# Optimization experiments

Measured on AMD Instinct MI355X. Metric: run time of the kernel, lower is better.

## Reference

```python
import jax, jax.numpy as jnp
import numpy as np


def _patch_points(P):
    # replicates: meshgrid(y,x,z, indexing='ij'); points = cat([zz, yy, xx], -1).reshape(-1,3)
    lin = jnp.linspace(-1.0, 1.0, P)
    a, b, c = jnp.meshgrid(lin, lin, lin, indexing='ij')  # all identical linspaces
    pts = jnp.stack([c, b, a], axis=-1).reshape(-1, 3)     # (P^3, 3)
    return pts


def _proj_locations(points, angles):
    # Tomographic projection geometry (generate_projections_location):
    # rotate points about the detector-vertical axis and keep in-plane coords.
    # points: (N,3); angles: (A,) radians. Returns (A, N, 2) grid coords (x, y)
    # in grid_sample convention (last dim: x indexes width, y indexes height).
    p0 = points[:, 0]
    p1 = points[:, 1]
    p2 = points[:, 2]
    c = jnp.cos(angles)[:, None]   # (A,1)
    s = jnp.sin(angles)[:, None]
    gx = p0[None, :] * c + p2[None, :] * s          # (A, N)
    gy = jnp.broadcast_to(p1[None, :], gx.shape)    # (A, N)
    return jnp.stack([gx, gy], axis=-1)             # (A, N, 2)


def _bilinear_sample(img, grid):
    # img: (C,H,W); grid: (N,2) in [-1,1], align_corners=True, padding zeros.
    C, H, W = img.shape
    ix = (grid[:, 0] + 1.0) * 0.5 * (W - 1)
    iy = (grid[:, 1] + 1.0) * 0.5 * (H - 1)
    ix0 = jnp.floor(ix)
    iy0 = jnp.floor(iy)
    ix1 = ix0 + 1.0
    iy1 = iy0 + 1.0
    wx1 = ix - ix0
    wx0 = 1.0 - wx1
    wy1 = iy - iy0
    wy0 = 1.0 - wy1

    def corner(iyc, ixc, w):
        valid = (ixc >= 0) & (ixc <= W - 1) & (iyc >= 0) & (iyc <= H - 1)
        xi = jnp.clip(ixc, 0, W - 1).astype(jnp.int32)
        yi = jnp.clip(iyc, 0, H - 1).astype(jnp.int32)
        return img[:, yi, xi] * (w * valid)[None, :]   # (C,N)

    return (corner(iy0, ix0, wy0 * wx0) + corner(iy0, ix1, wy0 * wx1)
            + corner(iy1, ix0, wy1 * wx0) + corner(iy1, ix1, wy1 * wx1))


def setup_inputs() -> dict:
    key = jax.random.key(0)
    k1, k2 = jax.random.split(key)
    B, A, P = 128, 121, 33
    x = jax.random.normal(k1, (B, A, P, P), dtype=jnp.float32)
    angles = jax.random.uniform(k2, (1, A), dtype=jnp.float32,
                                minval=0.0, maxval=2.0 * np.pi)
    return {"x": x, "angles": angles}


def reference(x, angles):
    B, A, P, _ = x.shape
    pts = _patch_points(P)                       # (P^3, 3)
    grids = _proj_locations(pts, angles[0])      # (A, P^3, 2)
    xs = jnp.transpose(x, (1, 0, 2, 3))          # (A, B, P, P)

    def body(acc, inp):
        xi, gi = inp                             # (B,P,P), (P^3,2)
        return acc + _bilinear_sample(xi, gi), None

    acc0 = jnp.zeros((B, P * P * P), dtype=x.dtype)
    acc, _ = jax.lax.scan(body, acc0, (xs, grids))
    x_fbp = acc.reshape(B, P, P, P) / A
    return x_fbp
```

## Files before the change

kernel.cpp:

```cpp
#include <hip/hip_runtime.h>
#include <hip/hip_fp16.h>
#include <math.h>


#define PDIM 33
#define PP   1089
#define A_   121
#define K_   3993
#define KP   4032
#define MP   1152
#define MT2  18
#define NT2  66
#define OUTB 35937

typedef _Float16 f16x8 __attribute__((ext_vector_type(8)));
typedef float    f32x4 __attribute__((ext_vector_type(4)));

typedef __attribute__((address_space(1))) const unsigned int* gp_t;
typedef __attribute__((address_space(3))) unsigned int*       lp_t;


__global__ __launch_bounds__(128)
void wfill_kernel(const float* __restrict__ angles, __half* __restrict__ W)
{
    const int n = blockIdx.x;
    const int t = threadIdx.x;
    __half* row = W + (size_t)n * KP;
    for (int e = t; e < KP; e += 128) row[e] = __float2half_rn(0.0f);
    __syncthreads();
    if (n >= PP || t >= A_) return;
    const int j  = t;
    const int i0 = n / PDIM;
    const int i2 = n - i0 * PDIM;
    float s, c;
    sincosf(angles[j], &s, &c);
    float ix = fmaf((float)(i2 - 16), c, fmaf((float)(i0 - 16), s, 16.0f));
    float fl = floorf(ix);
    int   k0 = (int)fl;
    float w1 = ix - fl;
    float w0 = 1.0f - w1;
    __half* seg = row + j * PDIM;
    if (k0 >= 0     && k0 < PDIM)     seg[k0]     = __float2half_rn(w0);
    if (k0 + 1 >= 0 && k0 + 1 < PDIM) seg[k0 + 1] = __float2half_rn(w1);
}

__global__ __launch_bounds__(256)
void xt_kernel(const float* __restrict__ x, __half* __restrict__ Xt)
{
    const int n  = blockIdx.x;
    const int i1 = n >> 7;
    const int b  = n & 127;
    const float* src = x + (size_t)b * (A_ * PP) + (size_t)i1 * PDIM;
    unsigned int* dst = (unsigned int*)(Xt + (size_t)n * KP);
    for (int e = threadIdx.x; e < KP / 2; e += 256) {
        int kk0 = 2 * e, kk1 = 2 * e + 1;
        float v0 = 0.0f, v1 = 0.0f;
        if (kk0 < K_) {
            int j = kk0 / PDIM, k = kk0 - j * PDIM;
            v0 = src[(size_t)j * PP + k];
        }
        if (kk1 < K_) {
            int j = kk1 / PDIM, k = kk1 - j * PDIM;
            v1 = src[(size_t)j * PP + k];
        }
        dst[e] = __builtin_bit_cast(unsigned int,
                     __builtin_amdgcn_cvt_pkrtz(v0, v1));
    }
}

__global__ __launch_bounds__(256)
void gemm_kernel(const __half* __restrict__ W, const __half* __restrict__ Xt,
                 float* __restrict__ out, float invA)
{
    __shared__ _Float16 As[64 * 64];
    __shared__ _Float16 Bs[64 * 64];

    const int blk   = blockIdx.x;
    const int tileN = blk / MT2;
    const int tileM = blk - tileN * MT2;
    const int t     = threadIdx.x;
    const int lane  = t & 63;
    const int wave  = t >> 6;
    const int warpM = wave >> 1;
    const int warpN = wave & 1;
    const int quad  = lane >> 4;
    const int l15   = lane & 15;

    f32x4 acc[2][2] = {};

    const __half* Ab = W  + (size_t)(tileM * 64) * KP;
    const __half* Bb = Xt + (size_t)(tileN * 64) * KP;

    int srow[2], ssego[2];
#pragma unroll
    for (int i = 0; i < 2; ++i) {
        int cidx = t + i * 256;
        int row  = cidx >> 3;
        int seg  = cidx & 7;
        srow[i]  = row;
        ssego[i] = (seg ^ (row & 7)) * 8;
    }

    int arow[2], brow[2];
#pragma unroll
    for (int s = 0; s < 2; ++s) {
        arow[s] = warpM * 32 + s * 16 + l15;
        brow[s] = warpN * 32 + s * 16 + l15;
    }

    for (int kb = 0; kb < KP; kb += 64) {
        __syncthreads();
#pragma unroll
        for (int i = 0; i < 2; ++i) {
            const __half* ga = Ab + (size_t)srow[i] * KP + kb + ssego[i];
            const __half* gb = Bb + (size_t)srow[i] * KP + kb + ssego[i];
            __builtin_amdgcn_global_load_lds((gp_t)(const void*)ga,
                (lp_t)(void*)&As[(t + i * 256) * 8], 16, 0, 0);
            __builtin_amdgcn_global_load_lds((gp_t)(const void*)gb,
                (lp_t)(void*)&Bs[(t + i * 256) * 8], 16, 0, 0);
        }
        __syncthreads();

        f16x8 af[2][2], bf[2][2];
#pragma unroll
        for (int h = 0; h < 2; ++h) {
#pragma unroll
            for (int s = 0; s < 2; ++s) {
                int ks = h * 4 + quad;
                af[h][s] = *(const f16x8*)&As[arow[s] * 64 + ((ks ^ (arow[s] & 7)) * 8)];
                bf[h][s] = *(const f16x8*)&Bs[brow[s] * 64 + ((ks ^ (brow[s] & 7)) * 8)];
            }
        }
#pragma unroll
        for (int h = 0; h < 2; ++h)
#pragma unroll
            for (int ms = 0; ms < 2; ++ms)
#pragma unroll
                for (int ns = 0; ns < 2; ++ns)
                    acc[ms][ns] = __builtin_amdgcn_mfma_f32_16x16x32_f16(
                        af[h][ms], bf[h][ns], acc[ms][ns], 0, 0, 0);
    }

#pragma unroll
    for (int ns = 0; ns < 2; ++ns) {
        int nglob = tileN * 64 + warpN * 32 + ns * 16 + l15;
        int i1 = nglob >> 7;
        int b  = nglob & 127;
        float* ob = out + (size_t)b * OUTB + (size_t)i1 * PDIM;
#pragma unroll
        for (int ms = 0; ms < 2; ++ms) {
#pragma unroll
            for (int r = 0; r < 4; ++r) {
                int m = tileM * 64 + warpM * 32 + ms * 16 + quad * 4 + r;
                if (m < PP) {
                    int i0 = m / PDIM;
                    int i2 = m - i0 * PDIM;
                    ob[(size_t)i0 * PP + i2] = acc[ms][ns][r] * invA;
                }
            }
        }
    }
}


#define ROWW 47
#define PADL 7
#define BLK  384
#define NV   3
#define GRID 1280

typedef _Float16 h2v __attribute__((ext_vector_type(2)));

#if defined(__has_builtin)
#if __has_builtin(__builtin_amdgcn_fractf)
#define FRACTF(x) __builtin_amdgcn_fractf(x)
#endif
#endif
#ifndef FRACTF
#define FRACTF(x) ((x) - floorf(x))
#endif

__device__ __forceinline__ float fdot2u(unsigned int a, unsigned int b, float c)
{
    return __builtin_amdgcn_fdot2(__builtin_bit_cast(h2v, a),
                                  __builtin_bit_cast(h2v, b), c, false);
}

__global__ __launch_bounds__(BLK)
void fbp_adjoint_kernel(const float* __restrict__ x,
                        const float* __restrict__ angles,
                        float* __restrict__ out,
                        int nslice, float invA)
{
    __shared__ unsigned int dr[A_ * ROWW];
    __shared__ float2       cs_lds[A_];

    const int t = threadIdx.x;
    for (int j = t; j < A_; j += BLK) {
        float s, c;
        sincosf(angles[j], &s, &c);
        cs_lds[j] = make_float2(c, s);
    }

    float u0[NV], u2[NV];
#pragma unroll
    for (int nn = 0; nn < NV; ++nn) {
        int n  = t + nn * BLK;
        int nc = (n < PP) ? n : (PP - 1);
        int q0 = nc / PDIM;
        int q2 = nc - q0 * PDIM;
        u0[nn] = (float)(q0 - 16);
        u2[nn] = (float)(q2 - 16);
    }

    for (int slice = blockIdx.x; slice < nslice; slice += GRID) {
        if (slice != (int)blockIdx.x) __syncthreads();
        const int hb = slice / PDIM;
        const int i1 = slice - hb * PDIM;
        const int b0 = 2 * hb;
        const float* r0 = x + (size_t)b0 * (A_ * PP) + (size_t)i1 * PDIM;
        const float* r1 = r0 + (size_t)(A_ * PP);
        for (int e = t; e < A_ * ROWW; e += BLK) {
            int j = e / ROWW;
            int p = e - j * ROWW;
            int k = p - PADL;
            float f0 = 0.0f, f1 = 0.0f;
            if (k >= 0 && k < PDIM) {
                size_t o = (size_t)j * PP + k;
                f0 = r0[o];
                f1 = r1[o];
            }
            dr[e] = __builtin_bit_cast(unsigned int,
                        __halves2half2(__float2half_rn(f0), __float2half_rn(f1)));
        }
        __syncthreads();

        float a0[NV] = {0.0f, 0.0f, 0.0f};
        float a1[NV] = {0.0f, 0.0f, 0.0f};
#pragma unroll 2
        for (int j = 0; j < A_; ++j) {
            float2 cj = cs_lds[j];
            const unsigned int* base = &dr[j * ROWW];
#pragma unroll
            for (int nn = 0; nn < NV; ++nn) {
                float ixp = fmaf(u2[nn], cj.x, fmaf(u0[nn], cj.y, 23.0f));
                int   kp  = (int)ixp;
                float w1  = FRACTF(ixp);
                unsigned int wp = __builtin_bit_cast(unsigned int,
                                    __builtin_amdgcn_cvt_pkrtz(1.0f - w1, w1));
                unsigned int d0 = base[kp];
                unsigned int d1 = base[kp + 1];
                unsigned int p0 = __builtin_amdgcn_perm(d1, d0, 0x05040100u);
                unsigned int p1 = __builtin_amdgcn_perm(d1, d0, 0x07060302u);
                a0[nn] = fdot2u(p0, wp, a0[nn]);
                a1[nn] = fdot2u(p1, wp, a1[nn]);
            }
        }

        float* ob0 = out + (size_t)b0 * OUTB + (size_t)i1 * PDIM;
        float* ob1 = ob0 + (size_t)OUTB;
#pragma unroll
        for (int nn = 0; nn < NV; ++nn) {
            int n = t + nn * BLK;
            if (n < PP) {
                int q0 = n / PDIM;
                int q2 = n - q0 * PDIM;
                size_t o = (size_t)q0 * PP + q2;
                ob0[o] = a0[nn] * invA;
                ob1[o] = a1[nn] * invA;
            }
        }
    }
}


extern "C" void kernel_launch(void* const* d_in, const int* in_sizes, int n_in,
                              void* d_out, int out_size, void* d_ws, size_t ws_size,
                              hipStream_t stream)
{
    const float* x      = (const float*)d_in[0];
    const float* angles = (const float*)d_in[1];
    float* out          = (float*)d_out;

    const int A = in_sizes[1];
    const int B = in_sizes[0] / (A * PP);
    const float invA = 1.0f / (float)A;

    const size_t wBytes  = (size_t)MP * KP * sizeof(__half);
    const size_t xtBytes = (size_t)(PDIM * B) * KP * sizeof(__half);

    if (ws_size >= wBytes + xtBytes && A == A_ && B == 128) {
        __half* W  = (__half*)d_ws;
        __half* Xt = (__half*)((char*)d_ws + wBytes);
        wfill_kernel<<<MP, 128, 0, stream>>>(angles, W);
        xt_kernel<<<PDIM * B, 256, 0, stream>>>(x, Xt);
        gemm_kernel<<<NT2 * MT2, 256, 0, stream>>>(W, Xt, out, invA);
    } else {
        const int nslice = (B / 2) * PDIM;
        dim3 grid(GRID < nslice ? GRID : nslice);
        fbp_adjoint_kernel<<<grid, BLK, 0, stream>>>(x, angles, out,
                                                     nslice, invA);
    }
}
```

Before: 191.5 us.

## Fuse prep kernels into one launch and swizzle GEMM tiles across XCDs

Merges the weight-fill and input-transpose kernels into a single prep launch, with 256 threads per block and zeroing done in 16-byte stores, which saves one launch and its gap. Remaps GEMM workgroup IDs so each XCD gets a contiguous group of tiles made of clusters sharing M/N rows, aiming for better L2 reuse of W and Xt. The mapping is hardcoded for 1188 workgroups split over 8 XCDs, which ties it to this problem shape.

```diff
diff --git a/kernel.cpp b/kernel.cpp
--- a/kernel.cpp
+++ b/kernel.cpp
@@ -11,6 +11,7 @@
 #define MP   1152
 #define MT2  18
 #define NT2  66
+#define NWG  1188
 #define OUTB 35937
 
 typedef _Float16 f16x8 __attribute__((ext_vector_type(8)));
@@ -20,51 +21,54 @@
 typedef __attribute__((address_space(3))) unsigned int*       lp_t;
 
 
-__global__ __launch_bounds__(128)
-void wfill_kernel(const float* __restrict__ angles, __half* __restrict__ W)
-{
-    const int n = blockIdx.x;
-    const int t = threadIdx.x;
-    __half* row = W + (size_t)n * KP;
-    for (int e = t; e < KP; e += 128) row[e] = __float2half_rn(0.0f);
-    __syncthreads();
-    if (n >= PP || t >= A_) return;
-    const int j  = t;
-    const int i0 = n / PDIM;
-    const int i2 = n - i0 * PDIM;
-    float s, c;
-    sincosf(angles[j], &s, &c);
-    float ix = fmaf((float)(i2 - 16), c, fmaf((float)(i0 - 16), s, 16.0f));
-    float fl = floorf(ix);
-    int   k0 = (int)fl;
-    float w1 = ix - fl;
-    float w0 = 1.0f - w1;
-    __half* seg = row + j * PDIM;
-    if (k0 >= 0     && k0 < PDIM)     seg[k0]     = __float2half_rn(w0);
-    if (k0 + 1 >= 0 && k0 + 1 < PDIM) seg[k0 + 1] = __float2half_rn(w1);
-}
-
 __global__ __launch_bounds__(256)
-void xt_kernel(const float* __restrict__ x, __half* __restrict__ Xt)
-{
-    const int n  = blockIdx.x;
-    const int i1 = n >> 7;
-    const int b  = n & 127;
-    const float* src = x + (size_t)b * (A_ * PP) + (size_t)i1 * PDIM;
-    unsigned int* dst = (unsigned int*)(Xt + (size_t)n * KP);
-    for (int e = threadIdx.x; e < KP / 2; e += 256) {
-        int kk0 = 2 * e, kk1 = 2 * e + 1;
-        float v0 = 0.0f, v1 = 0.0f;
-        if (kk0 < K_) {
-            int j = kk0 / PDIM, k = kk0 - j * PDIM;
-            v0 = src[(size_t)j * PP + k];
-        }
-        if (kk1 < K_) {
-            int j = kk1 / PDIM, k = kk1 - j * PDIM;
-            v1 = src[(size_t)j * PP + k];
-        }
-        dst[e] = __builtin_bit_cast(unsigned int,
-                     __builtin_amdgcn_cvt_pkrtz(v0, v1));
+void prep_kernel(const float* __restrict__ x, const float* __restrict__ angles,
+                 __half* __restrict__ Xt, __half* __restrict__ W)
+{
+    const int blk = blockIdx.x;
+    const int t   = threadIdx.x;
+
+    if (blk < PDIM * 128) {
+        const int n  = blk;
+        const int i1 = n >> 7;
+        const int b  = n & 127;
+        const float* src = x + (size_t)b * (A_ * PP) + (size_t)i1 * PDIM;
+        unsigned int* dst = (unsigned int*)(Xt + (size_t)n * KP);
+        for (int e = t; e < KP / 2; e += 256) {
+            int kk0 = 2 * e, kk1 = 2 * e + 1;
+            float v0 = 0.0f, v1 = 0.0f;
+            if (kk0 < K_) {
+                int j = kk0 / PDIM, k = kk0 - j * PDIM;
+                v0 = src[(size_t)j * PP + k];
+            }
+            if (kk1 < K_) {
+                int j = kk1 / PDIM, k = kk1 - j * PDIM;
+                v1 = src[(size_t)j * PP + k];
+            }
+            dst[e] = __builtin_bit_cast(unsigned int,
+                         __builtin_amdgcn_cvt_pkrtz(v0, v1));
+        }
+    } else {
+        const int n = blk - PDIM * 128;
+        __half* row = W + (size_t)n * KP;
+        int4 zz = make_int4(0, 0, 0, 0);
+        for (int e = t; e < KP / 8; e += 256)
+            ((int4*)row)[e] = zz;
+        __syncthreads();
+        if (n >= PP || t >= A_) return;
+        const int j  = t;
+        const int i0 = n / PDIM;
+        const int i2 = n - i0 * PDIM;
+        float s, c;
+        sincosf(angles[j], &s, &c);
+        float ix = fmaf((float)(i2 - 16), c, fmaf((float)(i0 - 16), s, 16.0f));
+        float fl = floorf(ix);
+        int   k0 = (int)fl;
+        float w1 = ix - fl;
+        float w0 = 1.0f - w1;
+        __half* seg = row + j * PDIM;
+        if (k0 >= 0     && k0 < PDIM)     seg[k0]     = __float2half_rn(w0);
+        if (k0 + 1 >= 0 && k0 + 1 < PDIM) seg[k0 + 1] = __float2half_rn(w1);
     }
 }
 
@@ -75,9 +79,23 @@
     __shared__ _Float16 As[64 * 64];
     __shared__ _Float16 Bs[64 * 64];
 
-    const int blk   = blockIdx.x;
-    const int tileN = blk / MT2;
-    const int tileM = blk - tileN * MT2;
+    const int b0  = blockIdx.x;
+    const int xcd = b0 & 7;
+    const int pos = b0 >> 3;
+    const int d   = (xcd < 4) ? xcd * 149 + pos
+                              : 596 + (xcd - 4) * 148 + pos;
+    int tileM, tileN;
+    if (d < 324) {
+        int c = d / 162, l = d - c * 162;
+        tileM = l / 9;
+        tileN = c * 9 + (l - tileM * 9);
+    } else {
+        int dd = d - 324;
+        int c = dd / 144, l = dd - c * 144;
+        tileM = l >> 3;
+        tileN = 18 + c * 8 + (l & 7);
+    }
+
     const int t     = threadIdx.x;
     const int lane  = t & 63;
     const int wave  = t >> 6;
@@ -292,9 +310,8 @@
     if (ws_size >= wBytes + xtBytes && A == A_ && B == 128) {
         __half* W  = (__half*)d_ws;
         __half* Xt = (__half*)((char*)d_ws + wBytes);
-        wfill_kernel<<<MP, 128, 0, stream>>>(angles, W);
-        xt_kernel<<<PDIM * B, 256, 0, stream>>>(x, Xt);
-        gemm_kernel<<<NT2 * MT2, 256, 0, stream>>>(W, Xt, out, invA);
+        prep_kernel<<<PDIM * B + MP, 256, 0, stream>>>(x, angles, Xt, W);
+        gemm_kernel<<<NWG, 256, 0, stream>>>(W, Xt, out, invA);
     } else {
         const int nslice = (B / 2) * PDIM;
         dim3 grid(GRID < nslice ? GRID : nslice);
```

After: 178.2 us. 6.9% less time.
